# Kernel tuning notes

Hardware: AMD Instinct MI355X
Metric: run time of the kernel (lower is better)

## Reference

```python
import jax, jax.numpy as jnp
import numpy as np

PATCH = 256
CH = 28


def setup_inputs() -> dict:
    key = jax.random.key(0)
    kx, km = jax.random.split(key)
    x = jax.random.normal(kx, (32, PATCH, PATCH, CH), dtype=jnp.float32)
    # bk: binary mask from a (P/2, P/2) random pattern, tiled 2x2, repeated over channels
    ms = PATCH // 2
    bk_fixed = jnp.round(jax.random.uniform(km, (ms, ms), dtype=jnp.float32))
    bk_tile = jnp.tile(bk_fixed, (2, 2))                      # [P, P]
    bk = jnp.repeat(bk_tile[:, :, None], CH, axis=2)          # [P, P, C]
    return {"x": x, "bk": bk}


def reference(x, bk):
    # Original math per channel ch:
    #   y[i,j,ch] = x[(i+ch)%P, j, ch] * bk[i,j,ch]      (roll by -ch, multiply)
    #   z[i,j,ch] = y[(i-ch)%P, j, ch]                   (roll back by +ch)
    # => z[i,j,ch] = x[i,j,ch] * bk[(i-ch)%P, j, ch]
    # So fuse the two rolls into a single per-channel roll of the mask,
    # then a fused multiply + channel-sum (single memory pass).
    C = x.shape[-1]
    shifts = jnp.arange(C)
    # roll each channel of the mask by +ch along height
    bk_shifted = jax.vmap(lambda m, s: jnp.roll(m, s, axis=0),
                          in_axes=(2, 0), out_axes=2)(bk, shifts)  # [P, P, C]
    # fused shift-multiply-accumulate: [B, P, P]
    return jnp.sum(x * bk_shifted[None], axis=-1)
```

## Files before the change

### kernel.cpp

```cpp
#include <hip/hip_runtime.h>

#define P 256
#define C 28
#define NPIX (P * P)
#define NIMG 32
#define Q 7
#define BLK 448
#define PIX 64
#define MROWS C
#define MPITCH 65
#define MTILE (MROWS * PIX)

__global__ __launch_bounds__(BLK) void codednet_kernel(
    const float4* __restrict__ x4, const float* __restrict__ bk,
    float* __restrict__ out) {
    __shared__ float sm[MROWS * MPITCH];
    __shared__ float sred[2][BLK];
    int t = threadIdx.x;
    int n = blockIdx.x;

    int xcd   = n & 7;
    int loc   = n >> 3;
    int i_loc = loc >> 2;
    int j0b   = loc & 3;
    int i     = (xcd << 5) + i_loc;
    int j0    = j0b << 6;
    int pix0  = (i << 8) + j0;

#pragma unroll
    for (int k = 0; k < MTILE / BLK; ++k) {
        int idx = t + k * BLK;
        int c   = idx >> 6;
        int col = idx & 63;
        int sr  = (i - c) & (P - 1);
        sm[c * MPITCH + col] = bk[((sr << 8) + j0 + col) * C + c];
    }
    __syncthreads();

    int pix_loc = t / 7;
    int q       = t - pix_loc * 7;
    int c0      = q << 2;
    float m0 = sm[(c0    ) * MPITCH + pix_loc];
    float m1 = sm[(c0 + 1) * MPITCH + pix_loc];
    float m2 = sm[(c0 + 2) * MPITCH + pix_loc];
    float m3 = sm[(c0 + 3) * MPITCH + pix_loc];

    const float4* xb = x4 + (size_t)pix0 * Q;
    float4 a = xb[t];
    for (int img = 0; img < NIMG; ++img) {
        float4 acur = a;
        if (img + 1 < NIMG)
            a = xb[(size_t)(img + 1) * (NPIX * Q) + t];
        sred[img & 1][t] = acur.x * m0 + acur.y * m1 + acur.z * m2 + acur.w * m3;
        __syncthreads();
        if (t < PIX) {
            const float* p = sred[img & 1] + t * Q;
            float acc = ((p[0] + p[1]) + (p[2] + p[3])) + ((p[4] + p[5]) + p[6]);
            out[img * NPIX + pix0 + t] = acc;
        }
    }
}

extern "C" void kernel_launch(void* const* d_in, const int* in_sizes, int n_in,
                              void* d_out, int out_size, void* d_ws, size_t ws_size,
                              hipStream_t stream) {
    const float4* x4 = (const float4*)d_in[0];
    const float* bk  = (const float*)d_in[1];
    float* out = (float*)d_out;
    codednet_kernel<<<P * (P / PIX), BLK, 0, stream>>>(x4, bk, out);
}
```

Before: 333.9 us.

## Replace shared-memory channel reduction with warp shuffle over 8-lane groups

Each pixel now maps to 8 lanes (7 active, 1 padding), and the per-pixel channel sum is done with xor shuffles instead of writing partials to shared memory and calling __syncthreads every image. This removes one block-wide barrier per image and the serial 64-thread reduction tail. In exchange, one eighth of the lanes idle and the block grows to 512 threads. The explicit register prefetch of the next image is replaced by unroll-4 to keep loads in flight.

```diff
diff --git a/kernel.cpp b/kernel.cpp
--- a/kernel.cpp
+++ b/kernel.cpp
@@ -5,17 +5,15 @@
 #define NPIX (P * P)
 #define NIMG 32
 #define Q 7
-#define BLK 448
+#define BLK 512
 #define PIX 64
-#define MROWS C
 #define MPITCH 65
-#define MTILE (MROWS * PIX)
+#define MTILE (C * PIX)
 
-__global__ __launch_bounds__(BLK) void codednet_kernel(
+__global__ __launch_bounds__(BLK) void codednet_shfl_kernel(
     const float4* __restrict__ x4, const float* __restrict__ bk,
     float* __restrict__ out) {
-    __shared__ float sm[MROWS * MPITCH];
-    __shared__ float sred[2][BLK];
+    __shared__ float sm[C * MPITCH];
     int t = threadIdx.x;
     int n = blockIdx.x;
 
@@ -27,9 +25,7 @@
     int j0    = j0b << 6;
     int pix0  = (i << 8) + j0;
 
-#pragma unroll
-    for (int k = 0; k < MTILE / BLK; ++k) {
-        int idx = t + k * BLK;
+    for (int idx = t; idx < MTILE; idx += BLK) {
         int c   = idx >> 6;
         int col = idx & 63;
         int sr  = (i - c) & (P - 1);
@@ -37,27 +33,30 @@
     }
     __syncthreads();
 
-    int pix_loc = t / 7;
-    int q       = t - pix_loc * 7;
+    int q       = t & 7;
+    int pix_loc = t >> 3;
     int c0      = q << 2;
-    float m0 = sm[(c0    ) * MPITCH + pix_loc];
-    float m1 = sm[(c0 + 1) * MPITCH + pix_loc];
-    float m2 = sm[(c0 + 2) * MPITCH + pix_loc];
-    float m3 = sm[(c0 + 3) * MPITCH + pix_loc];
 
-    const float4* xb = x4 + (size_t)pix0 * Q;
-    float4 a = xb[t];
+    float m0 = 0.f, m1 = 0.f, m2 = 0.f, m3 = 0.f;
+    if (q < 7) {
+        m0 = sm[(c0    ) * MPITCH + pix_loc];
+        m1 = sm[(c0 + 1) * MPITCH + pix_loc];
+        m2 = sm[(c0 + 2) * MPITCH + pix_loc];
+        m3 = sm[(c0 + 3) * MPITCH + pix_loc];
+    }
+
+    int fbase = (pix0 + pix_loc) * Q + q;
+    int obase = pix0 + pix_loc;
+
+#pragma unroll 4
     for (int img = 0; img < NIMG; ++img) {
-        float4 acur = a;
-        if (img + 1 < NIMG)
-            a = xb[(size_t)(img + 1) * (NPIX * Q) + t];
-        sred[img & 1][t] = acur.x * m0 + acur.y * m1 + acur.z * m2 + acur.w * m3;
-        __syncthreads();
-        if (t < PIX) {
-            const float* p = sred[img & 1] + t * Q;
-            float acc = ((p[0] + p[1]) + (p[2] + p[3])) + ((p[4] + p[5]) + p[6]);
-            out[img * NPIX + pix0 + t] = acc;
-        }
+        float4 a = make_float4(0.f, 0.f, 0.f, 0.f);
+        if (q < 7) a = x4[(size_t)img * (NPIX * Q) + fbase];
+        float acc = a.x * m0 + a.y * m1 + a.z * m2 + a.w * m3;
+        acc += __shfl_xor(acc, 1);
+        acc += __shfl_xor(acc, 2);
+        acc += __shfl_xor(acc, 4);
+        if (q == 0) out[img * NPIX + obase] = acc;
     }
 }
 
@@ -67,5 +66,5 @@
     const float4* x4 = (const float4*)d_in[0];
     const float* bk  = (const float*)d_in[1];
     float* out = (float*)d_out;
-    codednet_kernel<<<P * (P / PIX), BLK, 0, stream>>>(x4, bk, out);
+    codednet_shfl_kernel<<<P * (P / PIX), BLK, 0, stream>>>(x4, bk, out);
 }
```

New measurement: 324.0 us. 1.03x faster.
